# Kernel tuning notes

Measured on AMD Instinct MI355X. Metric: run time of the kernel, lower is better.

Reference implementation:

```python
import jax, jax.numpy as jnp
import numpy as np

B, T, D, K = 4, 4096, 1024, 64


def setup_inputs() -> dict:
    key = jax.random.key(0)
    k1, k2, k3, k4 = jax.random.split(key, 4)
    x = jax.random.normal(k1, (B, T, D), dtype=jnp.float32)
    Wq = jax.random.normal(k2, (D, K), dtype=jnp.float32) * (D ** -0.5)
    Wk = jax.random.normal(k3, (D, K), dtype=jnp.float32) * (D ** -0.5)
    Wv = jax.random.normal(k4, (D, D), dtype=jnp.float32) * (D ** -0.5)
    return {"x": x, "Wq": Wq, "Wk": Wk, "Wv": Wv}


def reference(x, Wq, Wk, Wv):
    # x: (B,T,D); single-head causal self-attention with value dim = D
    Bx, Tx, Dx = x.shape
    head_size = Wq.shape[-1]
    q = jnp.einsum('btd,dk->btk', x, Wq)  # (B,T,K)
    k = jnp.einsum('btd,dk->btk', x, Wk)  # (B,T,K)
    v = jnp.einsum('btd,de->bte', x, Wv)  # (B,T,D)
    scores = jnp.einsum('bqk,bsk->bqs', q, k) * (head_size ** -0.5)  # (B,T,T)
    causal = jnp.tril(jnp.ones((Tx, Tx), dtype=bool))
    scores = jnp.where(causal[None, :, :], scores, -jnp.inf)
    attn = jax.nn.softmax(scores, axis=-1)
    return jnp.einsum('bqs,bsd->bqd', attn, v)  # (B,T,D)
```

## Files before the change

### kernel.cpp

```cpp
#include <hip/hip_runtime.h>
#include <hip/hip_bf16.h>

typedef __attribute__((ext_vector_type(8))) short bf16x8;
typedef __attribute__((ext_vector_type(4))) float f32x4;
typedef unsigned short u16;

#define MFMA16(a, b, c) __builtin_amdgcn_mfma_f32_16x16x32_bf16((a), (b), (c), 0, 0, 0)
#define GLLDS(gp, lp)                                                                  \
  __builtin_amdgcn_global_load_lds((const __attribute__((address_space(1))) unsigned int*)(gp), \
                                   (__attribute__((address_space(3))) unsigned int*)(lp), 16, 0, 0)

__device__ __forceinline__ float fexp2(float x) { return __builtin_amdgcn_exp2f(x); }

__device__ __forceinline__ u16 f2b(float f) {
  union { float f; unsigned u; } x; x.f = f;
  return (u16)((x.u + 0x7FFFu + ((x.u >> 16) & 1u)) >> 16);
}
__device__ __forceinline__ unsigned f2b_hw(float f) {
  union { __hip_bfloat16 h; u16 u; } c;
  c.h = __float2bfloat16(f);
  return (unsigned)c.u;
}

__global__ __launch_bounds__(256) void k_cvt(const float* __restrict__ in,
                                             u16* __restrict__ out, int n4) {
  int i = blockIdx.x * 256 + threadIdx.x;
  if (i >= n4) return;
  float4 v = ((const float4*)in)[i];
  u16 a = f2b(v.x), b = f2b(v.y), c = f2b(v.z), d = f2b(v.w);
  ((uint2*)out)[i] = make_uint2((unsigned)a | ((unsigned)b << 16),
                                (unsigned)c | ((unsigned)d << 16));
}

__global__ __launch_bounds__(256) void k_packT(const float* __restrict__ in,
                                               u16* __restrict__ out, int R, int C) {
  __shared__ float t[32][33];
  int r0 = blockIdx.x * 32, c0 = blockIdx.y * 32;
  int cx = threadIdx.x & 31, ry = threadIdx.x >> 5;
#pragma unroll
  for (int k = 0; k < 4; k++)
    t[ry + k * 8][cx] = in[(size_t)(r0 + ry + k * 8) * C + c0 + cx];
  __syncthreads();
#pragma unroll
  for (int k = 0; k < 4; k++)
    out[(size_t)(c0 + ry + k * 8) * R + r0 + cx] = f2b(t[cx][ry + k * 8]);
}

__global__ __launch_bounds__(256) void k_gemm_qk(const u16* __restrict__ xb,
                                                 const u16* __restrict__ wqt,
                                                 const u16* __restrict__ wkt,
                                                 u16* __restrict__ q, u16* __restrict__ kk) {
  int row0 = blockIdx.x * 64;
  int tid = threadIdx.x, w = tid >> 6, l = tid & 63, l15 = l & 15, lg = l >> 4;
  const u16* wt = (w < 2) ? wqt : wkt;
  int nbase = (w & 1) * 32;
  f32x4 acc[4][2];
#pragma unroll
  for (int mt = 0; mt < 4; mt++)
#pragma unroll
    for (int nt = 0; nt < 2; nt++) acc[mt][nt] = (f32x4){0.f, 0.f, 0.f, 0.f};

  for (int k0 = 0; k0 < 1024; k0 += 32) {
    bf16x8 bfr[2], afr[4];
#pragma unroll
    for (int nt = 0; nt < 2; nt++)
      bfr[nt] = *(const bf16x8*)&wt[(size_t)(nbase + nt * 16 + l15) * 1024 + k0 + lg * 8];
#pragma unroll
    for (int mt = 0; mt < 4; mt++)
      afr[mt] = *(const bf16x8*)&xb[(size_t)(row0 + mt * 16 + l15) * 1024 + k0 + lg * 8];
#pragma unroll
    for (int mt = 0; mt < 4; mt++)
#pragma unroll
      for (int nt = 0; nt < 2; nt++) acc[mt][nt] = MFMA16(afr[mt], bfr[nt], acc[mt][nt]);
  }
  if (w < 2) {
#pragma unroll
    for (int mt = 0; mt < 4; mt++)
#pragma unroll
      for (int nt = 0; nt < 2; nt++)
#pragma unroll
        for (int j = 0; j < 4; j++)
          q[(size_t)(row0 + mt * 16 + lg * 4 + j) * 64 + nbase + nt * 16 + l15] =
              f2b(acc[mt][nt][j] * 0.18033688f);
  } else {
#pragma unroll
    for (int mt = 0; mt < 4; mt++)
#pragma unroll
      for (int nt = 0; nt < 2; nt++)
#pragma unroll
        for (int j = 0; j < 4; j++) {
          int row = row0 + mt * 16 + lg * 4 + j;
          int c = (nbase + nt * 16 + l15) * 2;
          size_t off = (size_t)(row >> 6) * 8192 + (row & 63) * 128 + (c ^ ((row & 7) << 4));
          *(u16*)((char*)kk + off) = f2b(acc[mt][nt][j]);
        }
  }
}

__global__ __launch_bounds__(256) void k_gemm_v(const u16* __restrict__ xb,
                                                const u16* __restrict__ wvt,
                                                u16* __restrict__ vT) {
  int b = blockIdx.z;
  int d0 = blockIdx.y * 128;
  int s0 = blockIdx.x * 128;
  int tid = threadIdx.x, w = tid >> 6, l = tid & 63, l15 = l & 15, lg = l >> 4;
  int wd = (w & 1) * 64, wsn = (w >> 1) * 64;
  __shared__ __align__(16) char lds[32768];

  const u16* arow = wvt + (size_t)d0 * 1024;
  const u16* brow = xb + (size_t)(b * 4096 + s0) * 1024;

  auto stage = [&](int buf, int k0) {
    char* La = lds + buf * 16384;
    char* Lb = La + 8192;
#pragma unroll
    for (int i = 0; i < 2; i++) {
      int row = w * 32 + i * 16 + (l >> 2), kq = (l & 3) * 8;
      GLLDS(&arow[(size_t)row * 1024 + k0 + kq], La + (w * 2 + i) * 1024);
      GLLDS(&brow[(size_t)row * 1024 + k0 + kq], Lb + (w * 2 + i) * 1024);
    }
  };

  f32x4 acc[4][4];
#pragma unroll
  for (int mt = 0; mt < 4; mt++)
#pragma unroll
    for (int nt = 0; nt < 4; nt++) acc[mt][nt] = (f32x4){0.f, 0.f, 0.f, 0.f};

  stage(0, 0);
  __syncthreads();
  int buf = 0;
  for (int k = 0; k < 32; k++) {
    if (k < 31) stage(buf ^ 1, (k + 1) * 32);
    const char* La = lds + buf * 16384;
    const char* Lb = La + 8192;
    bf16x8 afr[4], bfr[4];
#pragma unroll
    for (int mt = 0; mt < 4; mt++)
      afr[mt] = *(const bf16x8*)(La + (wd + mt * 16 + l15) * 64 + lg * 16);
#pragma unroll
    for (int nt = 0; nt < 4; nt++)
      bfr[nt] = *(const bf16x8*)(Lb + (wsn + nt * 16 + l15) * 64 + lg * 16);
    __builtin_amdgcn_s_setprio(1);
#pragma unroll
    for (int mt = 0; mt < 4; mt++)
#pragma unroll
      for (int nt = 0; nt < 4; nt++) acc[mt][nt] = MFMA16(afr[mt], bfr[nt], acc[mt][nt]);
    __builtin_amdgcn_s_setprio(0);
    __syncthreads();
    buf ^= 1;
  }
#pragma unroll
  for (int mt = 0; mt < 4; mt++)
#pragma unroll
    for (int nt = 0; nt < 4; nt++)
#pragma unroll
      for (int j = 0; j < 4; j++) {
        int d = d0 + wd + mt * 16 + lg * 4 + j;
        int s = s0 + wsn + nt * 16 + l15;
        size_t off = ((size_t)(b * 64 + (s >> 6)) * 8 + (d >> 7)) * 16384 + (d & 127) * 128 +
                     (((s & 63) * 2) ^ ((d & 7) << 4));
        *(u16*)((char*)vT + off) = f2b(acc[mt][nt][j]);
      }
}

__global__ __launch_bounds__(512, 2) void k_attn(const u16* __restrict__ qw,
                                                 const u16* __restrict__ kws,
                                                 const u16* __restrict__ vts,
                                                 float* __restrict__ out) {
  int bid = blockIdx.x;
  int xcd = bid & 7, r = bid >> 3;
  int cmb = r & 1, q5 = r >> 1;
  int half = q5 >> 4, idx = q5 & 15;
  int p = half ? 31 - idx : idx;
  int g = xcd * 2 + cmb;
  int cpair = g & 3, b = g >> 2;
  int tid = threadIdx.x, w = tid >> 6, l = tid & 63, l15 = l & 15, lg = l >> 4;
  int sw = (l15 & 7) << 4;
  size_t tokb = (size_t)b * 4096;

  __shared__ __align__(16) char lds[66560];
  char* Pb = lds + 49152;
  float* scb = (float*)(lds + 65536);
  float* lb = (float*)(lds + 66048);

  auto stageV = [&](int t) {
    const char* vb = (const char*)vts + ((size_t)(b * 64 + t) * 8 + cpair * 2) * 16384;
    char* lv = lds + 16384;
#pragma unroll
    for (int i = 0; i < 4; i++) {
      int s = w * 4 + i;
      GLLDS(vb + s * 1024 + l * 16, lv + s * 1024);
    }
  };
  auto stageK = [&](int t, int bufi) {
    const char* kb = (const char*)kws + (size_t)(b * 64 + t) * 8192;
    GLLDS(kb + w * 1024 + l * 16, lds + bufi * 8192 + w * 1024);
  };

  int Q0 = p * 128;
  int ntb = (Q0 >> 6) + 2;
  int qsA = Q0 + w * 16;
  int qA = qsA + l15;
  int qpos = w & 1, dq = w >> 1;
  int qsB = Q0 + qpos * 64;

  bf16x8 qf[2];
#pragma unroll
  for (int ks = 0; ks < 2; ks++)
    qf[ks] = *(const bf16x8*)&qw[(tokb + qA) * 64 + ks * 32 + lg * 8];

  f32x4 acc[4][4];
  float mrow = -1e30f, Lrun = 0.f;
#pragma unroll
  for (int mt = 0; mt < 4; mt++)
#pragma unroll
    for (int qt = 0; qt < 4; qt++) acc[mt][qt] = (f32x4){0.f, 0.f, 0.f, 0.f};

  stageK(0, 0);
  __syncthreads();
  int buf = 0;
  for (int t = 0; t < ntb; t++) {
    int s0 = t * 64;
    stageV(t);
    if (t + 1 < ntb) stageK(t + 1, buf ^ 1);
    if (s0 < qsA + 16) {
      const char* Kb = lds + buf * 8192;
      f32x4 sfr[4];
      __builtin_amdgcn_s_setprio(1);
#pragma unroll
      for (int nt = 0; nt < 4; nt++) {
        const char* kr = Kb + (nt * 16 + l15) * 128;
        bf16x8 kf0 = *(const bf16x8*)(kr + ((lg * 16) ^ sw));
        bf16x8 kf1 = *(const bf16x8*)(kr + ((64 + lg * 16) ^ sw));
        f32x4 z = (f32x4){0.f, 0.f, 0.f, 0.f};
        z = MFMA16(kf0, qf[0], z);
        sfr[nt] = MFMA16(kf1, qf[1], z);
      }
      __builtin_amdgcn_s_setprio(0);
      if (s0 + 63 > qsA) {
#pragma unroll
        for (int nt = 0; nt < 4; nt++)
#pragma unroll
          for (int j = 0; j < 4; j++)
            if (s0 + nt * 16 + lg * 4 + j > qA) sfr[nt][j] = -1e30f;
      }
      float pm = fmaxf(fmaxf(fmaxf(sfr[0][0], sfr[0][1]), fmaxf(sfr[0][2], sfr[0][3])),
                       fmaxf(fmaxf(sfr[1][0], sfr[1][1]), fmaxf(sfr[1][2], sfr[1][3])));
      pm = fmaxf(pm, fmaxf(fmaxf(fmaxf(sfr[2][0], sfr[2][1]), fmaxf(sfr[2][2], sfr[2][3])),
                           fmaxf(fmaxf(sfr[3][0], sfr[3][1]), fmaxf(sfr[3][2], sfr[3][3]))));
      pm = fmaxf(pm, __shfl_xor(pm, 16));
      pm = fmaxf(pm, __shfl_xor(pm, 32));
      float sc = 1.0f;
      if (__any(pm > mrow + 11.54f)) {
        float mn = fmaxf(mrow, pm);
        sc = fexp2(mrow - mn);
        mrow = mn;
      }
      int rq = w * 16 + l15;
      scb[rq] = sc;
      int rbase = rq * 128, sx = (rq & 7) << 4;
      float psum = 0.f;
#pragma unroll
      for (int nt = 0; nt < 4; nt++) {
        unsigned u0 = f2b_hw(fexp2(sfr[nt][0] - mrow));
        unsigned u1 = f2b_hw(fexp2(sfr[nt][1] - mrow));
        unsigned u2 = f2b_hw(fexp2(sfr[nt][2] - mrow));
        unsigned u3 = f2b_hw(fexp2(sfr[nt][3] - mrow));
        psum += __uint_as_float(u0 << 16) + __uint_as_float(u1 << 16) +
                __uint_as_float(u2 << 16) + __uint_as_float(u3 << 16);
        int addr = (rbase + (nt * 16 + lg * 4) * 2) ^ sx;
        *(uint2*)(Pb + addr) = make_uint2(u0 | (u1 << 16), u2 | (u3 << 16));
      }
      psum += __shfl_xor(psum, 16);
      psum += __shfl_xor(psum, 32);
      Lrun = Lrun * sc + psum;
      if (lg == 0) lb[rq] = Lrun;
    }
    __syncthreads();
    if (s0 < qsB + 64) {
      int qlo = (s0 - qsB) >> 4;
      if (qlo < 0) qlo = 0;
      const char* Vb = lds + 16384 + (dq >> 1) * 16384;
      int drow = (dq & 1) * 64;
      bf16x8 pf[4][2];
#pragma unroll
      for (int qt = 0; qt < 4; qt++)
        if (qt >= qlo) {
          int R = qpos * 64 + qt * 16 + l15;
          float sq = scb[R];
          if (!__all(sq == 1.0f)) {
#pragma unroll
            for (int mt = 0; mt < 4; mt++) acc[mt][qt] *= sq;
          }
          int rx = (R & 7) << 4;
          pf[qt][0] = *(const bf16x8*)(Pb + ((R * 128 + lg * 16) ^ rx));
          pf[qt][1] = *(const bf16x8*)(Pb + ((R * 128 + 64 + lg * 16) ^ rx));
        }
      __builtin_amdgcn_s_setprio(1);
#pragma unroll
      for (int mt = 0; mt < 4; mt++) {
        const char* vr = Vb + (drow + mt * 16 + l15) * 128;
        bf16x8 va0 = *(const bf16x8*)(vr + ((lg * 16) ^ sw));
        bf16x8 va1 = *(const bf16x8*)(vr + ((64 + lg * 16) ^ sw));
#pragma unroll
        for (int qt = 0; qt < 4; qt++)
          if (qt >= qlo) {
            acc[mt][qt] = MFMA16(va0, pf[qt][0], acc[mt][qt]);
            acc[mt][qt] = MFMA16(va1, pf[qt][1], acc[mt][qt]);
          }
      }
      __builtin_amdgcn_s_setprio(0);
    }
    __syncthreads();
    buf ^= 1;
  }
#pragma unroll
  for (int qt = 0; qt < 4; qt++) {
    float linv = 1.0f / lb[qpos * 64 + qt * 16 + l15];
#pragma unroll
    for (int mt = 0; mt < 4; mt++) {
      f32x4 v = acc[mt][qt] * linv;
      size_t o = (tokb + qsB + qt * 16 + l15) * 1024 + cpair * 256 + dq * 64 +
                 mt * 16 + lg * 4;
      *(f32x4*)&out[o] = v;
    }
  }
}

extern "C" void kernel_launch(void* const* d_in, const int* in_sizes, int n_in,
                              void* d_out, int out_size, void* d_ws, size_t ws_size,
                              hipStream_t stream) {
  const float* x  = (const float*)d_in[0];
  const float* Wq = (const float*)d_in[1];
  const float* Wk = (const float*)d_in[2];
  const float* Wv = (const float*)d_in[3];
  float* out = (float*)d_out;
  char* ws = (char*)d_ws;
  u16* xb  = (u16*)(ws);
  u16* qw  = (u16*)(ws + 33554432);
  u16* kw  = (u16*)(ws + 35651584);
  u16* vT  = (u16*)(ws + 37748736);
  u16* wqt = (u16*)(ws + 71303168);
  u16* wkt = (u16*)(ws + 71434240);
  u16* wvt = (u16*)(ws + 71565312);

  k_cvt<<<16384, 256, 0, stream>>>(x, xb, 4194304);
  k_packT<<<dim3(32, 2), 256, 0, stream>>>(Wq, wqt, 1024, 64);
  k_packT<<<dim3(32, 2), 256, 0, stream>>>(Wk, wkt, 1024, 64);
  k_packT<<<dim3(32, 32), 256, 0, stream>>>(Wv, wvt, 1024, 1024);
  k_gemm_qk<<<256, 256, 0, stream>>>(xb, wqt, wkt, qw, kw);
  k_gemm_v<<<dim3(32, 8, 4), 256, 0, stream>>>(xb, wvt, vT);
  k_attn<<<512, 512, 0, stream>>>(qw, kw, vT, out);
}
```

Measured before the change: 234.9 us.

## Compute softmax row sums with MFMA against ones and drop causal branch in PV

The per-row softmax denominator is no longer built from scalar adds and cross-lane shuffles in the score phase. Each wave instead accumulates it in the PV phase with an extra pair of MFMAs that multiply a vector of bf16 ones by the P tile, rescaled alongside the output accumulators. The qlo-based skipping of fully masked q-tiles in the PV loop is replaced by zero-filled P fragments, so all MFMAs run unconditionally and the inner loop has no branches. This removes VALU and shuffle work from the softmax path, at the cost of extra MFMAs on masked tiles, two additional MFMAs per step, and one more barrier at the end.

```diff
diff --git a/kernel.cpp b/kernel.cpp
--- a/kernel.cpp
+++ b/kernel.cpp
@@ -184,6 +184,10 @@
   float* scb = (float*)(lds + 65536);
   float* lb = (float*)(lds + 66048);
 
+  const short ob = (short)0x3F80;
+  const bf16x8 ones = {ob, ob, ob, ob, ob, ob, ob, ob};
+  const bf16x8 zf = {0, 0, 0, 0, 0, 0, 0, 0};
+
   auto stageV = [&](int t) {
     const char* vb = (const char*)vts + ((size_t)(b * 64 + t) * 8 + cpair * 2) * 16384;
     char* lv = lds + 16384;
@@ -211,11 +215,13 @@
     qf[ks] = *(const bf16x8*)&qw[(tokb + qA) * 64 + ks * 32 + lg * 8];
 
   f32x4 acc[4][4];
-  float mrow = -1e30f, Lrun = 0.f;
+  f32x4 accl;
+  float mrow = -1e30f;
 #pragma unroll
   for (int mt = 0; mt < 4; mt++)
 #pragma unroll
     for (int qt = 0; qt < 4; qt++) acc[mt][qt] = (f32x4){0.f, 0.f, 0.f, 0.f};
+  accl = (f32x4){0.f, 0.f, 0.f, 0.f};
 
   stageK(0, 0);
   __syncthreads();
@@ -260,43 +266,56 @@
       int rq = w * 16 + l15;
       scb[rq] = sc;
       int rbase = rq * 128, sx = (rq & 7) << 4;
-      float psum = 0.f;
 #pragma unroll
       for (int nt = 0; nt < 4; nt++) {
-        unsigned u0 = f2b_hw(fexp2(sfr[nt][0] - mrow));
-        unsigned u1 = f2b_hw(fexp2(sfr[nt][1] - mrow));
-        unsigned u2 = f2b_hw(fexp2(sfr[nt][2] - mrow));
-        unsigned u3 = f2b_hw(fexp2(sfr[nt][3] - mrow));
-        psum += __uint_as_float(u0 << 16) + __uint_as_float(u1 << 16) +
-                __uint_as_float(u2 << 16) + __uint_as_float(u3 << 16);
+        unsigned lo = f2b_hw(fexp2(sfr[nt][0] - mrow)) |
+                      (f2b_hw(fexp2(sfr[nt][1] - mrow)) << 16);
+        unsigned hi2 = f2b_hw(fexp2(sfr[nt][2] - mrow)) |
+                       (f2b_hw(fexp2(sfr[nt][3] - mrow)) << 16);
         int addr = (rbase + (nt * 16 + lg * 4) * 2) ^ sx;
-        *(uint2*)(Pb + addr) = make_uint2(u0 | (u1 << 16), u2 | (u3 << 16));
-      }
-      psum += __shfl_xor(psum, 16);
-      psum += __shfl_xor(psum, 32);
-      Lrun = Lrun * sc + psum;
-      if (lg == 0) lb[rq] = Lrun;
+        *(uint2*)(Pb + addr) = make_uint2(lo, hi2);
+      }
     }
     __syncthreads();
     if (s0 < qsB + 64) {
-      int qlo = (s0 - qsB) >> 4;
-      if (qlo < 0) qlo = 0;
       const char* Vb = lds + 16384 + (dq >> 1) * 16384;
       int drow = (dq & 1) * 64;
       bf16x8 pf[4][2];
-#pragma unroll
-      for (int qt = 0; qt < 4; qt++)
-        if (qt >= qlo) {
-          int R = qpos * 64 + qt * 16 + l15;
-          float sq = scb[R];
-          if (!__all(sq == 1.0f)) {
-#pragma unroll
-            for (int mt = 0; mt < 4; mt++) acc[mt][qt] *= sq;
-          }
+      float sq[4];
+#pragma unroll
+      for (int qt = 0; qt < 4; qt++) {
+        int R = qpos * 64 + qt * 16 + l15;
+        bool act = s0 < qsB + qt * 16 + 16;
+        sq[qt] = act ? scb[R] : 1.0f;
+        if (act) {
           int rx = (R & 7) << 4;
           pf[qt][0] = *(const bf16x8*)(Pb + ((R * 128 + lg * 16) ^ rx));
           pf[qt][1] = *(const bf16x8*)(Pb + ((R * 128 + 64 + lg * 16) ^ rx));
-        }
+        } else {
+          pf[qt][0] = zf;
+          pf[qt][1] = zf;
+        }
+      }
+#pragma unroll
+      for (int qt = 0; qt < 4; qt++)
+        if (!__all(sq[qt] == 1.0f)) {
+#pragma unroll
+          for (int mt = 0; mt < 4; mt++) acc[mt][qt] *= sq[qt];
+        }
+      {
+        int Rl = qpos * 64 + dq * 16 + l15;
+        bool actl = s0 < qsB + dq * 16 + 16;
+        float sql = actl ? scb[Rl] : 1.0f;
+        if (!__all(sql == 1.0f)) accl *= sql;
+        bf16x8 pl0 = zf, pl1 = zf;
+        if (actl) {
+          int rx = (Rl & 7) << 4;
+          pl0 = *(const bf16x8*)(Pb + ((Rl * 128 + lg * 16) ^ rx));
+          pl1 = *(const bf16x8*)(Pb + ((Rl * 128 + 64 + lg * 16) ^ rx));
+        }
+        accl = MFMA16(ones, pl0, accl);
+        accl = MFMA16(ones, pl1, accl);
+      }
       __builtin_amdgcn_s_setprio(1);
 #pragma unroll
       for (int mt = 0; mt < 4; mt++) {
@@ -304,17 +323,18 @@
         bf16x8 va0 = *(const bf16x8*)(vr + ((lg * 16) ^ sw));
         bf16x8 va1 = *(const bf16x8*)(vr + ((64 + lg * 16) ^ sw));
 #pragma unroll
-        for (int qt = 0; qt < 4; qt++)
-          if (qt >= qlo) {
-            acc[mt][qt] = MFMA16(va0, pf[qt][0], acc[mt][qt]);
-            acc[mt][qt] = MFMA16(va1, pf[qt][1], acc[mt][qt]);
-          }
+        for (int qt = 0; qt < 4; qt++) {
+          acc[mt][qt] = MFMA16(va0, pf[qt][0], acc[mt][qt]);
+          acc[mt][qt] = MFMA16(va1, pf[qt][1], acc[mt][qt]);
+        }
       }
       __builtin_amdgcn_s_setprio(0);
     }
     __syncthreads();
     buf ^= 1;
   }
+  if (lg == 0) lb[qpos * 64 + dq * 16 + l15] = accl[0];
+  __syncthreads();
 #pragma unroll
   for (int qt = 0; qt < 4; qt++) {
     float linv = 1.0f / lb[qpos * 64 + qt * 16 + l15];
```

New measurement: 231.4 us. Within noise of the previous version (-1.5%).
